# Optimization experiments

Hardware: AMD Instinct MI355X
Metric: run time of the kernel (lower is better)

Reference implementation:

```python
import jax, jax.numpy as jnp
import numpy as np
from jax import lax

WIRES = 4
EPS = 1e-5


def _conv2d(x, w, b):
    # x: [B,C,H,W], w: [O,I,3,3], SAME padding, stride 1
    y = lax.conv_general_dilated(x, w, (1, 1), 'SAME',
                                 dimension_numbers=('NCHW', 'OIHW', 'NCHW'))
    return y + b[None, :, None, None]


def _maxpool2(x):
    return lax.reduce_window(x, -jnp.inf, lax.max, (1, 1, 2, 2), (1, 1, 2, 2), 'VALID')


def _cnot_perm(c, t, n=WIRES):
    # wire 0 = most significant bit; CNOT is a self-inverse basis permutation
    idx = np.arange(2 ** n)
    cbit = (idx >> (n - 1 - c)) & 1
    flipped = idx ^ (1 << (n - 1 - t))
    return np.where(cbit == 1, flipped, idx)


_CNOT_PERMS = [_cnot_perm(c, c + 1) for c in range(WIRES - 1)]
_Z_SIGNS = np.stack([1.0 - 2.0 * ((np.arange(2 ** WIRES) >> (WIRES - 1 - i)) & 1)
                     for i in range(WIRES)], axis=1).astype(np.float32)  # [16, 4]


def _quantum_circuit(q_params, feats):
    # Batched state-vector sim of: RY(feats[i]) wire i; RX(params[i]) wire i;
    # CNOT chain; <Z_i>.  feats: [B,4], q_params: [4]
    hf = 0.5 * feats
    hp = 0.5 * q_params
    cy, sy = jnp.cos(hf), jnp.sin(hf)            # [B,4]
    cx, sx = jnp.cos(hp), jnp.sin(hp)            # [4]
    # per-wire state after RX @ RY |0>: amplitudes of |0>, |1>
    a0 = (cx * cy - 1j * sx * sy).astype(jnp.complex64)  # [B,4]
    a1 = (cx * sy - 1j * sx * cy).astype(jnp.complex64)  # [B,4]
    single = jnp.stack([a0, a1], axis=-1)        # [B,4,2]
    # product state -> full 16-dim state via successive outer products
    psi = single[:, 0]                           # [B,2]
    for i in range(1, WIRES):
        psi = (psi[:, :, None] * single[:, i][:, None, :]).reshape(psi.shape[0], -1)
    # CNOT chain = fixed basis permutations
    for perm in _CNOT_PERMS:
        psi = psi[:, perm]                       # [B,16]
    probs = psi.real ** 2 + psi.imag ** 2        # [B,16]
    return probs @ jnp.asarray(_Z_SIGNS)         # [B,4]


def setup_inputs() -> dict:
    key = jax.random.key(0)
    ks = jax.random.split(key, 8)
    B, C, H, W = 512, 1, 128, 128
    return {
        'x': jax.random.normal(ks[0], (B, C, H, W), jnp.float32),
        'conv1_w': jax.random.normal(ks[1], (8, C, 3, 3), jnp.float32) * 0.1,
        'conv1_b': jnp.zeros((8,), jnp.float32),
        'conv2_w': jax.random.normal(ks[2], (16, 8, 3, 3), jnp.float32) * 0.1,
        'conv2_b': jnp.zeros((16,), jnp.float32),
        'q_params': jax.random.normal(ks[3], (WIRES,), jnp.float32),
        'bn_gamma': jnp.ones((4,), jnp.float32),
        'bn_beta': jnp.zeros((4,), jnp.float32),
        'head_w': jax.random.normal(ks[4], (4, WIRES), jnp.float32) * 0.5,
        'head_b': jnp.zeros((4,), jnp.float32),
    }


def reference(x, conv1_w, conv1_b, conv2_w, conv2_b, q_params,
              bn_gamma, bn_beta, head_w, head_b):
    h = jax.nn.relu(_conv2d(x, conv1_w, conv1_b))
    h = _maxpool2(h)
    h = jax.nn.relu(_conv2d(h, conv2_w, conv2_b))
    h = _maxpool2(h)
    feats = h.mean(axis=(2, 3))                  # AdaptiveAvgPool2d(1) -> [B,16]
    q_out = _quantum_circuit(q_params, feats[:, :WIRES])  # [B,4]
    # BatchNorm1d (training mode, biased variance)
    mu = q_out.mean(axis=0)
    var = q_out.var(axis=0)
    normed = bn_gamma * (q_out - mu) / jnp.sqrt(var + EPS) + bn_beta
    return normed @ head_w.T + head_b
```

## Files before the change

### kernel.cpp

```cpp
#include <hip/hip_runtime.h>

#define EPS 1e-5f

typedef float f2 __attribute__((ext_vector_type(2)));
typedef float f4 __attribute__((ext_vector_type(4)));

__device__ __forceinline__ float uload(const float* __restrict__ p) {
  return __int_as_float(__builtin_amdgcn_readfirstlane(__float_as_int(*p)));
}

__device__ __forceinline__ f2 fma2(f2 a, f2 b, f2 c) {
  return __builtin_elementwise_fma(a, b, c);
}
__device__ __forceinline__ f2 splat2(float s) { f2 r; r.x = s; r.y = s; return r; }

__global__ __launch_bounds__(256, 4) void k12_fused(
    const float* __restrict__ x, const float* __restrict__ w1,
    const float* __restrict__ b1, const float* __restrict__ w2,
    const float* __restrict__ b2, float* __restrict__ partials) {
  __shared__ float p1[8][18][66];
  __shared__ float w1t[80];
  __shared__ float w2t[292];
  __shared__ float wred[4][4];

  const int q   = blockIdx.x & 3;
  const int b   = blockIdx.x >> 2;
  const int tid = threadIdx.x;
  const float* xb = x + (size_t)b * (128 * 128);

  auto c1_load = [&](int pos, float xin[4][6]) {
    const int gl = pos >> 5, i = pos & 31;
    const int G  = 16 * q - 1 + gl;
    const bool vG = ((unsigned)G) < 64u;
    const int xr0 = 2 * G - 1;
#pragma unroll
    for (int r = 0; r < 4; ++r) {
      const int row  = xr0 + r;
      const bool rok = vG && ((unsigned)row < 128u);
      const int rowc = min(max(row, 0), 127);
      const float* rp = xb + rowc * 128;
      const float le = rp[(i == 0) ? 0 : (4 * i - 1)];
      const f4 mid   = *(const f4*)(rp + 4 * i);
      const float ri = rp[(i == 31) ? 127 : (4 * i + 4)];
      xin[r][0] = (rok && i != 0)  ? le    : 0.f;
      xin[r][1] = rok              ? mid.x : 0.f;
      xin[r][2] = rok              ? mid.y : 0.f;
      xin[r][3] = rok              ? mid.z : 0.f;
      xin[r][4] = rok              ? mid.w : 0.f;
      xin[r][5] = (rok && i != 31) ? ri    : 0.f;
    }
  };
  auto c1_compute = [&](int pos, const float xin[4][6]) {
    const int gl = pos >> 5, i = pos & 31;
    const int G  = 16 * q - 1 + gl;
    const bool vG = ((unsigned)G) < 64u;
#pragma unroll 1
    for (int g = 0; g < 2; ++g) {
      f2 wpx[9][2], bias1[2];
#pragma unroll
      for (int k = 0; k < 9; ++k) {
        wpx[k][0] = *(const f2*)&w1t[k * 8 + 4 * g];
        wpx[k][1] = *(const f2*)&w1t[k * 8 + 4 * g + 2];
      }
      bias1[0] = *(const f2*)&w1t[72 + 4 * g];
      bias1[1] = *(const f2*)&w1t[72 + 4 * g + 2];
#pragma unroll
      for (int p = 0; p < 2; ++p)
#pragma unroll
        for (int h = 0; h < 2; ++h) {
          f2 best = splat2(0.f);
#pragma unroll
          for (int dy = 0; dy < 2; ++dy)
#pragma unroll
            for (int dx = 0; dx < 2; ++dx) {
              f2 a = bias1[p];
#pragma unroll
              for (int ky = 0; ky < 3; ++ky)
#pragma unroll
                for (int kx = 0; kx < 3; ++kx)
                  a = fma2(wpx[ky * 3 + kx][p],
                           splat2(xin[dy + ky][2 * h + dx + kx]), a);
              best.x = fmaxf(best.x, a.x);
              best.y = fmaxf(best.y, a.y);
            }
          const int oc0 = 4 * g + 2 * p;
          p1[oc0][gl][2 * i + 1 + h]     = vG ? best.x : 0.f;
          p1[oc0 + 1][gl][2 * i + 1 + h] = vG ? best.y : 0.f;
        }
    }
  };

  if (tid < 72) {
    int oc = tid / 9, k = tid % 9;
    w1t[k * 8 + oc] = w1[tid];
  } else if (tid < 80) {
    w1t[tid] = b1[tid - 72];
  }
  {
    int t = tid;
    {
      int oc = t / 72, rem = t % 72, ic = rem / 9, k = rem % 9;
      w2t[(ic * 9 + k) * 4 + oc] = w2[t];
    }
    t = tid + 256;
    if (t < 288) {
      int oc = t / 72, rem = t % 72, ic = rem / 9, k = rem % 9;
      w2t[(ic * 9 + k) * 4 + oc] = w2[t];
    }
  }
  if (tid >= 80 && tid < 84) w2t[288 + tid - 80] = b2[tid - 80];
  if (tid >= 96 && tid < 240) {
    int t = tid - 96;
    int ic = t / 18, r = t % 18;
    p1[ic][r][0]  = 0.f;
    p1[ic][r][65] = 0.f;
  }

  float xin0[4][6];
  c1_load(tid, xin0);
  __syncthreads();

  c1_compute(tid, xin0);
#pragma unroll 1
  for (int pos = tid + 256; pos < 576; pos += 256) {
    float xin[4][6];
    c1_load(pos, xin);
    c1_compute(pos, xin);
  }
  __syncthreads();

  const int px2  = tid & 31;
  const int py2l = tid >> 5;

  f2 acc[2][2][2];
#pragma unroll
  for (int p = 0; p < 2; ++p) {
    const f2 bias = *(const f2*)&w2t[288 + 2 * p];
    acc[p][0][0] = bias; acc[p][0][1] = bias;
    acc[p][1][0] = bias; acc[p][1][1] = bias;
  }

#pragma unroll 1
  for (int ic = 0; ic < 8; ++ic) {
    float xin[4][4];
#pragma unroll
    for (int r = 0; r < 4; ++r) {
      const f2* rp = (const f2*)&p1[ic][2 * py2l + r][2 * px2];
      f2 v0 = rp[0], v1 = rp[1];
      xin[r][0] = v0.x; xin[r][1] = v0.y; xin[r][2] = v1.x; xin[r][3] = v1.y;
    }
#pragma unroll
    for (int ky = 0; ky < 3; ++ky)
#pragma unroll
      for (int kx = 0; kx < 3; ++kx) {
        const int k = ky * 3 + kx;
        const f2 w0  = *(const f2*)&w2t[(ic * 9 + k) * 4];
        const f2 w1p = *(const f2*)&w2t[(ic * 9 + k) * 4 + 2];
#pragma unroll
        for (int dy = 0; dy < 2; ++dy)
#pragma unroll
          for (int dx = 0; dx < 2; ++dx) {
            const f2 xs = splat2(xin[dy + ky][dx + kx]);
            acc[0][dy][dx] = fma2(w0, xs, acc[0][dy][dx]);
            acc[1][dy][dx] = fma2(w1p, xs, acc[1][dy][dx]);
          }
      }
  }

  const int lane = tid & 63, w = tid >> 6;
#pragma unroll
  for (int p = 0; p < 2; ++p) {
    f2 m01;
    m01.x = fmaxf(fmaxf(fmaxf(acc[p][0][0].x, acc[p][0][1].x),
                        fmaxf(acc[p][1][0].x, acc[p][1][1].x)), 0.f);
    m01.y = fmaxf(fmaxf(fmaxf(acc[p][0][0].y, acc[p][0][1].y),
                        fmaxf(acc[p][1][0].y, acc[p][1][1].y)), 0.f);
#pragma unroll
    for (int off = 32; off > 0; off >>= 1) {
      m01.x += __shfl_down(m01.x, off);
      m01.y += __shfl_down(m01.y, off);
    }
    if (lane == 0) { wred[w][2 * p] = m01.x; wred[w][2 * p + 1] = m01.y; }
  }
  __syncthreads();
  if (tid < 4) {
    float s = wred[0][tid] + wred[1][tid] + wred[2][tid] + wred[3][tid];
    partials[((size_t)b * 4 + q) * 4 + tid] = s;
  }
}

__global__ __launch_bounds__(512) void k3_tail(
    const float* __restrict__ partials, const float* __restrict__ qp,
    const float* __restrict__ gamma, const float* __restrict__ beta,
    const float* __restrict__ hw, const float* __restrict__ hb,
    float* __restrict__ out) {
  __shared__ float wsum[8][8];
  __shared__ float stats[8];
  const int tid = threadIdx.x;

  const f4* pp = (const f4*)(partials + tid * 16);
  f4 s0 = pp[0], s1 = pp[1], s2 = pp[2], s3 = pp[3];
  float f[4];
  f[0] = (s0.x + s1.x + s2.x + s3.x) * (1.f / 1024.f);
  f[1] = (s0.y + s1.y + s2.y + s3.y) * (1.f / 1024.f);
  f[2] = (s0.z + s1.z + s2.z + s3.z) * (1.f / 1024.f);
  f[3] = (s0.w + s1.w + s2.w + s3.w) * (1.f / 1024.f);

  float a0r[4], a0i[4], a1r[4], a1i[4];
#pragma unroll
  for (int i = 0; i < 4; ++i) {
    float cy, sy, cx, sx;
    __sincosf(0.5f * f[i], &sy, &cy);
    __sincosf(0.5f * uload(qp + i), &sx, &cx);
    a0r[i] = cx * cy; a0i[i] = -sx * sy;
    a1r[i] = cx * sy; a1i[i] = -sx * cy;
  }

  float pr[16], pi[16];
#pragma unroll
  for (int j = 0; j < 16; ++j) {
    float rr = 1.f, ii = 0.f;
#pragma unroll
    for (int w = 0; w < 4; ++w) {
      int bit = (j >> (3 - w)) & 1;
      float ar = bit ? a1r[w] : a0r[w];
      float ai = bit ? a1i[w] : a0i[w];
      float t = rr * ar - ii * ai;
      ii = rr * ai + ii * ar;
      rr = t;
    }
    pr[j] = rr; pi[j] = ii;
  }

  constexpr int comp[16] = {0, 1, 3, 2, 6, 7, 5, 4, 12, 13, 15, 14, 10, 11, 9, 8};
  float qv[4] = {0.f, 0.f, 0.f, 0.f};
#pragma unroll
  for (int j = 0; j < 16; ++j) {
    int s = comp[j];
    float p = pr[s] * pr[s] + pi[s] * pi[s];
#pragma unroll
    for (int i = 0; i < 4; ++i)
      qv[i] += ((j >> (3 - i)) & 1) ? -p : p;
  }

  float v[8];
#pragma unroll
  for (int i = 0; i < 4; ++i) { v[i] = qv[i]; v[4 + i] = qv[i] * qv[i]; }
#pragma unroll
  for (int k = 0; k < 8; ++k)
#pragma unroll
    for (int off = 32; off > 0; off >>= 1) v[k] += __shfl_down(v[k], off);
  const int lane = tid & 63, w = tid >> 6;
  if (lane == 0) {
#pragma unroll
    for (int k = 0; k < 8; ++k) wsum[w][k] = v[k];
  }
  __syncthreads();
  if (tid < 8) {
    float s = 0.f;
#pragma unroll
    for (int ww = 0; ww < 8; ++ww) s += wsum[ww][tid];
    stats[tid] = s * (1.f / 512.f);
  }
  __syncthreads();

  float nm[4];
#pragma unroll
  for (int i = 0; i < 4; ++i) {
    float mu  = stats[i];
    float var = stats[4 + i] - mu * mu;
    nm[i] = uload(gamma + i) * (qv[i] - mu) * rsqrtf(var + EPS) + uload(beta + i);
  }
#pragma unroll
  for (int k = 0; k < 4; ++k) {
    float o = uload(hb + k);
#pragma unroll
    for (int i = 0; i < 4; ++i) o = fmaf(nm[i], uload(hw + k * 4 + i), o);
    out[tid * 4 + k] = o;
  }
}

extern "C" void kernel_launch(void* const* d_in, const int* in_sizes, int n_in,
                              void* d_out, int out_size, void* d_ws, size_t ws_size,
                              hipStream_t stream) {
  const float* x  = (const float*)d_in[0];
  const float* w1 = (const float*)d_in[1];
  const float* b1 = (const float*)d_in[2];
  const float* w2 = (const float*)d_in[3];
  const float* b2 = (const float*)d_in[4];
  const float* qp = (const float*)d_in[5];
  const float* gm = (const float*)d_in[6];
  const float* bt = (const float*)d_in[7];
  const float* hw = (const float*)d_in[8];
  const float* hb = (const float*)d_in[9];
  float* out = (float*)d_out;

  float* partials = (float*)d_ws;

  k12_fused<<<512 * 4, 256, 0, stream>>>(x, w1, b1, w2, b2, partials);
  k3_tail<<<1, 512, 0, stream>>>(partials, qp, gm, bt, hw, hb, out);
}
```

Before: 120.3 us.

## Software-pipeline conv1 global loads and conv2 LDS loads, vectorize weight reads

The conv1 stage now issues the next position's vectorized global row loads before computing the current one, and unrolls the three position iterations. Conv2 double-buffers LDS input tiles across input channels so the next channel's loads overlap the current channel's FMAs. Weight reads become 16-byte aligned f4 LDS loads. This aims to hide global and LDS latency, at the cost of more live registers, which could reduce occupancy under the 256x4 launch bounds.

```diff
diff --git a/kernel.cpp b/kernel.cpp
--- a/kernel.cpp
+++ b/kernel.cpp
@@ -18,9 +18,9 @@
     const float* __restrict__ x, const float* __restrict__ w1,
     const float* __restrict__ b1, const float* __restrict__ w2,
     const float* __restrict__ b2, float* __restrict__ partials) {
-  __shared__ float p1[8][18][66];
-  __shared__ float w1t[80];
-  __shared__ float w2t[292];
+  __shared__ __align__(16) float p1[8][18][66];
+  __shared__ __align__(16) float w1t[80];
+  __shared__ __align__(16) float w2t[292];
   __shared__ float wred[4][4];
 
   const int q   = blockIdx.x & 3;
@@ -28,11 +28,23 @@
   const int tid = threadIdx.x;
   const float* xb = x + (size_t)b * (128 * 128);
 
-  auto c1_load = [&](int pos, float xin[4][6]) {
+  auto c1_load_mid = [&](int pos, f4 xm[4]) {
+    const int gl = pos >> 5, i = pos & 31;
+    const int G  = 16 * q - 1 + gl;
+    const int xr0 = 2 * G - 1;
+#pragma unroll
+    for (int r = 0; r < 4; ++r) {
+      const int rowc = min(max(xr0 + r, 0), 127);
+      xm[r] = *(const f4*)(xb + rowc * 128 + 4 * i);
+    }
+  };
+
+  auto c1_compute = [&](int pos, const f4 xm[4]) {
     const int gl = pos >> 5, i = pos & 31;
     const int G  = 16 * q - 1 + gl;
     const bool vG = ((unsigned)G) < 64u;
     const int xr0 = 2 * G - 1;
+    float xin[4][6];
 #pragma unroll
     for (int r = 0; r < 4; ++r) {
       const int row  = xr0 + r;
@@ -40,30 +52,21 @@
       const int rowc = min(max(row, 0), 127);
       const float* rp = xb + rowc * 128;
       const float le = rp[(i == 0) ? 0 : (4 * i - 1)];
-      const f4 mid   = *(const f4*)(rp + 4 * i);
       const float ri = rp[(i == 31) ? 127 : (4 * i + 4)];
-      xin[r][0] = (rok && i != 0)  ? le    : 0.f;
-      xin[r][1] = rok              ? mid.x : 0.f;
-      xin[r][2] = rok              ? mid.y : 0.f;
-      xin[r][3] = rok              ? mid.z : 0.f;
-      xin[r][4] = rok              ? mid.w : 0.f;
-      xin[r][5] = (rok && i != 31) ? ri    : 0.f;
-    }
-  };
-  auto c1_compute = [&](int pos, const float xin[4][6]) {
-    const int gl = pos >> 5, i = pos & 31;
-    const int G  = 16 * q - 1 + gl;
-    const bool vG = ((unsigned)G) < 64u;
+      xin[r][0] = (rok && i != 0)  ? le      : 0.f;
+      xin[r][1] = rok              ? xm[r].x : 0.f;
+      xin[r][2] = rok              ? xm[r].y : 0.f;
+      xin[r][3] = rok              ? xm[r].z : 0.f;
+      xin[r][4] = rok              ? xm[r].w : 0.f;
+      xin[r][5] = (rok && i != 31) ? ri      : 0.f;
+    }
 #pragma unroll 1
     for (int g = 0; g < 2; ++g) {
-      f2 wpx[9][2], bias1[2];
-#pragma unroll
-      for (int k = 0; k < 9; ++k) {
-        wpx[k][0] = *(const f2*)&w1t[k * 8 + 4 * g];
-        wpx[k][1] = *(const f2*)&w1t[k * 8 + 4 * g + 2];
-      }
-      bias1[0] = *(const f2*)&w1t[72 + 4 * g];
-      bias1[1] = *(const f2*)&w1t[72 + 4 * g + 2];
+      f4 wq[9];
+#pragma unroll
+      for (int k = 0; k < 9; ++k) wq[k] = *(const f4*)&w1t[k * 8 + 4 * g];
+      const f4 b4 = *(const f4*)&w1t[72 + 4 * g];
+      const f2 bias0 = b4.xy, bias1 = b4.zw;
 #pragma unroll
       for (int p = 0; p < 2; ++p)
 #pragma unroll
@@ -73,13 +76,14 @@
           for (int dy = 0; dy < 2; ++dy)
 #pragma unroll
             for (int dx = 0; dx < 2; ++dx) {
-              f2 a = bias1[p];
+              f2 a = p ? bias1 : bias0;
 #pragma unroll
               for (int ky = 0; ky < 3; ++ky)
 #pragma unroll
-                for (int kx = 0; kx < 3; ++kx)
-                  a = fma2(wpx[ky * 3 + kx][p],
-                           splat2(xin[dy + ky][2 * h + dx + kx]), a);
+                for (int kx = 0; kx < 3; ++kx) {
+                  const f2 wp = p ? wq[ky * 3 + kx].zw : wq[ky * 3 + kx].xy;
+                  a = fma2(wp, splat2(xin[dy + ky][2 * h + dx + kx]), a);
+                }
               best.x = fmaxf(best.x, a.x);
               best.y = fmaxf(best.y, a.y);
             }
@@ -116,17 +120,18 @@
     p1[ic][r][65] = 0.f;
   }
 
-  float xin0[4][6];
-  c1_load(tid, xin0);
-  __syncthreads();
-
-  c1_compute(tid, xin0);
-#pragma unroll 1
-  for (int pos = tid + 256; pos < 576; pos += 256) {
-    float xin[4][6];
-    c1_load(pos, xin);
-    c1_compute(pos, xin);
-  }
+  f4 xm0[4];
+  c1_load_mid(tid, xm0);
+  __syncthreads();
+
+  f4 xm1[4];
+  c1_load_mid(tid + 256, xm1);
+  c1_compute(tid, xm0);
+  const bool t3 = tid < 64;
+  f4 xm2[4];
+  if (t3) c1_load_mid(tid + 512, xm2);
+  c1_compute(tid + 256, xm1);
+  if (t3) c1_compute(tid + 512, xm2);
   __syncthreads();
 
   const int px2  = tid & 31;
@@ -140,31 +145,41 @@
     acc[p][1][0] = bias; acc[p][1][1] = bias;
   }
 
-#pragma unroll 1
-  for (int ic = 0; ic < 8; ++ic) {
-    float xin[4][4];
+  auto ld_xin = [&](int ic, float xin[4][4]) {
 #pragma unroll
     for (int r = 0; r < 4; ++r) {
       const f2* rp = (const f2*)&p1[ic][2 * py2l + r][2 * px2];
       f2 v0 = rp[0], v1 = rp[1];
       xin[r][0] = v0.x; xin[r][1] = v0.y; xin[r][2] = v1.x; xin[r][3] = v1.y;
     }
+  };
+  auto c2_acc = [&](int ic, const float xin[4][4]) {
 #pragma unroll
     for (int ky = 0; ky < 3; ++ky)
 #pragma unroll
       for (int kx = 0; kx < 3; ++kx) {
         const int k = ky * 3 + kx;
-        const f2 w0  = *(const f2*)&w2t[(ic * 9 + k) * 4];
-        const f2 w1p = *(const f2*)&w2t[(ic * 9 + k) * 4 + 2];
+        const f4 wv = *(const f4*)&w2t[(ic * 9 + k) * 4];
+        const f2 wA = wv.xy, wB = wv.zw;
 #pragma unroll
         for (int dy = 0; dy < 2; ++dy)
 #pragma unroll
           for (int dx = 0; dx < 2; ++dx) {
             const f2 xs = splat2(xin[dy + ky][dx + kx]);
-            acc[0][dy][dx] = fma2(w0, xs, acc[0][dy][dx]);
-            acc[1][dy][dx] = fma2(w1p, xs, acc[1][dy][dx]);
+            acc[0][dy][dx] = fma2(wA, xs, acc[0][dy][dx]);
+            acc[1][dy][dx] = fma2(wB, xs, acc[1][dy][dx]);
           }
       }
+  };
+
+  float xina[4][4], xinb[4][4];
+  ld_xin(0, xina);
+#pragma unroll 1
+  for (int ic = 0; ic < 8; ic += 2) {
+    ld_xin(ic + 1, xinb);
+    c2_acc(ic, xina);
+    if (ic < 6) ld_xin(ic + 2, xina);
+    c2_acc(ic + 1, xinb);
   }
 
   const int lane = tid & 63, w = tid >> 6;
```

Measured after the change: 124.3 us. 3.4% more time.
